# Kernel tuning notes

Measured on AMD Instinct MI355X. Metric: run time of the kernel, lower is better.

Reference implementation:

```python
import jax, jax.numpy as jnp
import numpy as np


def setup_inputs() -> dict:
    key = jax.random.key(0)
    k1, k2 = jax.random.split(key)
    B, H, S, D = 2, 16, 2048, 64
    scores = jax.random.normal(k1, (B, H, S, S), dtype=jnp.float32)
    v = jax.random.normal(k2, (B, H, S, D), dtype=jnp.float32)
    return {"scores": scores, "v": v}


def reference(scores, v):
    # softmax over last dim of [B,H,S,S], then contract with V [B,H,S,D]
    prob = jax.nn.softmax(scores, axis=-1)
    return jnp.einsum('bhqk,bhkd->bhqd', prob, v)
```

## Files before the change

kernel.cpp:

```cpp
#include <hip/hip_runtime.h>
#include <hip/hip_bf16.h>

#define NBH  32
#define SEQ  2048
#define DIM  64
#define PSTR 2056

typedef __attribute__((ext_vector_type(4))) float f32x4;
typedef __attribute__((ext_vector_type(8))) short bf16x8;

__device__ __forceinline__ unsigned short bfbits(float f) {
    unsigned u = __builtin_bit_cast(unsigned, f);
    u += 0x7FFFu + ((u >> 16) & 1u);
    return (unsigned short)(u >> 16);
}
__device__ __forceinline__ unsigned pk(float a, float b) {
    return (unsigned)bfbits(a) | ((unsigned)bfbits(b) << 16);
}

__global__ __launch_bounds__(512, 2)
void softmaxv_kernel(const float* __restrict__ scores,
                     const float* __restrict__ v,
                     float* __restrict__ out)
{
    __shared__ unsigned short P[16 * PSTR];
    __shared__ float red[4][64][8];

    const int tid  = threadIdx.x;
    const int w    = tid >> 6;
    const int lane = tid & 63;
    const int dt   = w & 3;
    const int ksub = w >> 2;
    const int g    = lane >> 4;
    const int c    = lane & 15;

    const int bid = blockIdx.x;
    const int bh  = bid & 31;
    const int s   = bid >> 5;

    const float* sblk = scores + ((size_t)bh * SEQ + s * 256) * SEQ;
    float* const oblk = out + ((size_t)bh * SEQ + s * 256) * DIM;

    bf16x8 ones;
#pragma unroll
    for (int j = 0; j < 8; ++j) ones[j] = (short)0x3F80;

    const int r0 = 2 * w;
    f32x4 st[2][8];

#define SEG(t, rr, j)                                                          \
    (*reinterpret_cast<const f32x4*>(                                          \
        sblk + (size_t)((t) * 16 + r0 + (rr)) * SEQ + (j) * 256 + (lane << 2)))

#define LDS_BAR asm volatile("s_waitcnt lgkmcnt(0)\n\ts_barrier" ::: "memory");

#pragma unroll
    for (int j = 0; j < 8; ++j) { st[0][j] = SEG(0, 0, j); st[1][j] = SEG(0, 1, j); }

    const float* vsrc = v + (size_t)bh * SEQ * DIM + dt * 16 + c;
    bf16x8 vreg[32];
#pragma unroll
    for (int kk = 0; kk < 32; ++kk) {
        bf16x8 f;
#pragma unroll
        for (int j = 0; j < 8; ++j)
            f[j] = (short)bfbits(vsrc[(size_t)(ksub * 1024 + kk * 32 + g * 8 + j) * DIM]);
        vreg[kk] = f;
    }

    for (int t = 0; t < 16; ++t) {
#pragma unroll
        for (int j = 0; j < 8; ++j) {
            const f32x4 sv0 = st[0][j];
            const f32x4 sv1 = st[1][j];
            if (t < 15) {
                st[0][j] = SEG(t + 1, 0, j);
                st[1][j] = SEG(t + 1, 1, j);
            }
            const float a0 = __expf(sv0[0]), a1 = __expf(sv0[1]);
            const float a2 = __expf(sv0[2]), a3 = __expf(sv0[3]);
            const float b0 = __expf(sv1[0]), b1 = __expf(sv1[1]);
            const float b2 = __expf(sv1[2]), b3 = __expf(sv1[3]);
            *reinterpret_cast<uint2*>(&P[r0 * PSTR + j * 256 + lane * 4]) =
                make_uint2(pk(a0, a1), pk(a2, a3));
            *reinterpret_cast<uint2*>(&P[(r0 + 1) * PSTR + j * 256 + lane * 4]) =
                make_uint2(pk(b0, b1), pk(b2, b3));
        }

        LDS_BAR

        f32x4 acc  = (f32x4)0.0f;
        f32x4 accl = (f32x4)0.0f;
#pragma unroll
        for (int kk = 0; kk < 32; ++kk) {
            const int K = ksub * 32 + kk;
            const bf16x8 a = *reinterpret_cast<const bf16x8*>(
                &P[c * PSTR + K * 32 + g * 8]);
            acc  = __builtin_amdgcn_mfma_f32_16x16x32_bf16(a, vreg[kk], acc,  0, 0, 0);
            accl = __builtin_amdgcn_mfma_f32_16x16x32_bf16(a, ones,     accl, 0, 0, 0);
        }

        if (ksub == 1) {
            *reinterpret_cast<f32x4*>(&red[dt][lane][0]) = acc;
            *reinterpret_cast<f32x4*>(&red[dt][lane][4]) = accl;
        }

        LDS_BAR

        if (ksub == 0) {
            const f32x4 a2 = *reinterpret_cast<const f32x4*>(&red[dt][lane][0]);
            const f32x4 l2 = *reinterpret_cast<const f32x4*>(&red[dt][lane][4]);
            const f32x4 at = acc + a2;
            const f32x4 lt = accl + l2;
            float* op = oblk + (size_t)(t * 16) * DIM + dt * 16 + c;
#pragma unroll
            for (int r = 0; r < 4; ++r)
                op[(size_t)(g * 4 + r) * DIM] = at[r] * (1.0f / lt[r]);
        }
    }
#undef SEG
#undef LDS_BAR
}

extern "C" void kernel_launch(void* const* d_in, const int* in_sizes, int n_in,
                              void* d_out, int out_size, void* d_ws, size_t ws_size,
                              hipStream_t stream)
{
    const float* scores = (const float*)d_in[0];
    const float* v      = (const float*)d_in[1];
    float* out          = (float*)d_out;

    softmaxv_kernel<<<dim3(256), dim3(512), 0, stream>>>(scores, v, out);
}
```

Baseline: 114.2 us.

## Double-buffer score loads two tiles ahead with ping-pong register windows

Score prefetch goes from one tile ahead to two tiles ahead, using two register windows (stA/stB) that alternate in a loop unrolled by two. Each window's next load is issued after its pack and barrier, so global loads overlap both the MFMA phase and the next pack. Launch bounds drop to one block per CU so the extra 32 float4 registers fit, which halves occupancy in exchange for deeper memory-level parallelism within each wave.

```diff
diff --git a/kernel.cpp b/kernel.cpp
--- a/kernel.cpp
+++ b/kernel.cpp
@@ -18,7 +18,7 @@
     return (unsigned)bfbits(a) | ((unsigned)bfbits(b) << 16);
 }
 
-__global__ __launch_bounds__(512, 2)
+__global__ __launch_bounds__(512, 1)
 void softmaxv_kernel(const float* __restrict__ scores,
                      const float* __restrict__ v,
                      float* __restrict__ out)
@@ -46,16 +46,71 @@
     for (int j = 0; j < 8; ++j) ones[j] = (short)0x3F80;
 
     const int r0 = 2 * w;
-    f32x4 st[2][8];
+    f32x4 stA[2][8], stB[2][8];
 
 #define SEG(t, rr, j)                                                          \
     (*reinterpret_cast<const f32x4*>(                                          \
         sblk + (size_t)((t) * 16 + r0 + (rr)) * SEQ + (j) * 256 + (lane << 2)))
 
+#define ISSUE_WIN(dst, t)                                                      \
+    {                                                                          \
+        _Pragma("unroll")                                                      \
+        for (int j = 0; j < 8; ++j) {                                          \
+            dst[0][j] = SEG(t, 0, j);                                          \
+            dst[1][j] = SEG(t, 1, j);                                          \
+        }                                                                      \
+    }
+
 #define LDS_BAR asm volatile("s_waitcnt lgkmcnt(0)\n\ts_barrier" ::: "memory");
 
-#pragma unroll
-    for (int j = 0; j < 8; ++j) { st[0][j] = SEG(0, 0, j); st[1][j] = SEG(0, 1, j); }
+#define PACK(src)                                                              \
+    {                                                                          \
+        _Pragma("unroll")                                                      \
+        for (int j = 0; j < 8; ++j) {                                          \
+            const f32x4 sv0 = src[0][j];                                       \
+            const f32x4 sv1 = src[1][j];                                       \
+            const float a0 = __expf(sv0[0]), a1 = __expf(sv0[1]);              \
+            const float a2 = __expf(sv0[2]), a3 = __expf(sv0[3]);              \
+            const float b0 = __expf(sv1[0]), b1 = __expf(sv1[1]);              \
+            const float b2 = __expf(sv1[2]), b3 = __expf(sv1[3]);              \
+            *reinterpret_cast<uint2*>(&P[r0 * PSTR + j * 256 + lane * 4]) =    \
+                make_uint2(pk(a0, a1), pk(a2, a3));                            \
+            *reinterpret_cast<uint2*>(&P[(r0 + 1) * PSTR + j * 256 + lane * 4]) = \
+                make_uint2(pk(b0, b1), pk(b2, b3));                            \
+        }                                                                      \
+    }
+
+#define MFMA_EPI(t)                                                            \
+    {                                                                          \
+        f32x4 acc  = (f32x4)0.0f;                                              \
+        f32x4 accl = (f32x4)0.0f;                                              \
+        _Pragma("unroll")                                                      \
+        for (int kk = 0; kk < 32; ++kk) {                                      \
+            const int K = ksub * 32 + kk;                                      \
+            const bf16x8 a = *reinterpret_cast<const bf16x8*>(                 \
+                &P[c * PSTR + K * 32 + g * 8]);                                \
+            acc  = __builtin_amdgcn_mfma_f32_16x16x32_bf16(a, vreg[kk], acc,  0, 0, 0); \
+            accl = __builtin_amdgcn_mfma_f32_16x16x32_bf16(a, ones,     accl, 0, 0, 0); \
+        }                                                                      \
+        if (ksub == 1) {                                                       \
+            *reinterpret_cast<f32x4*>(&red[dt][lane][0]) = acc;                \
+            *reinterpret_cast<f32x4*>(&red[dt][lane][4]) = accl;               \
+        }                                                                      \
+        LDS_BAR                                                                \
+        if (ksub == 0) {                                                       \
+            const f32x4 a2 = *reinterpret_cast<const f32x4*>(&red[dt][lane][0]); \
+            const f32x4 l2 = *reinterpret_cast<const f32x4*>(&red[dt][lane][4]); \
+            const f32x4 at = acc + a2;                                         \
+            const f32x4 lt = accl + l2;                                        \
+            float* op = oblk + (size_t)((t) * 16) * DIM + dt * 16 + c;         \
+            _Pragma("unroll")                                                  \
+            for (int r = 0; r < 4; ++r)                                        \
+                op[(size_t)(g * 4 + r) * DIM] = at[r] * (1.0f / lt[r]);        \
+        }                                                                      \
+    }
+
+    ISSUE_WIN(stA, 0)
+    ISSUE_WIN(stB, 1)
 
     const float* vsrc = v + (size_t)bh * SEQ * DIM + dt * 16 + c;
     bf16x8 vreg[32];
@@ -68,58 +123,22 @@
         vreg[kk] = f;
     }
 
-    for (int t = 0; t < 16; ++t) {
-#pragma unroll
-        for (int j = 0; j < 8; ++j) {
-            const f32x4 sv0 = st[0][j];
-            const f32x4 sv1 = st[1][j];
-            if (t < 15) {
-                st[0][j] = SEG(t + 1, 0, j);
-                st[1][j] = SEG(t + 1, 1, j);
-            }
-            const float a0 = __expf(sv0[0]), a1 = __expf(sv0[1]);
-            const float a2 = __expf(sv0[2]), a3 = __expf(sv0[3]);
-            const float b0 = __expf(sv1[0]), b1 = __expf(sv1[1]);
-            const float b2 = __expf(sv1[2]), b3 = __expf(sv1[3]);
-            *reinterpret_cast<uint2*>(&P[r0 * PSTR + j * 256 + lane * 4]) =
-                make_uint2(pk(a0, a1), pk(a2, a3));
-            *reinterpret_cast<uint2*>(&P[(r0 + 1) * PSTR + j * 256 + lane * 4]) =
-                make_uint2(pk(b0, b1), pk(b2, b3));
-        }
+    for (int t = 0; t < 16; t += 2) {
+        PACK(stA)
+        LDS_BAR
+        if (t + 2 < 16) ISSUE_WIN(stA, t + 2)
+        MFMA_EPI(t)
 
+        PACK(stB)
         LDS_BAR
-
-        f32x4 acc  = (f32x4)0.0f;
-        f32x4 accl = (f32x4)0.0f;
-#pragma unroll
-        for (int kk = 0; kk < 32; ++kk) {
-            const int K = ksub * 32 + kk;
-            const bf16x8 a = *reinterpret_cast<const bf16x8*>(
-                &P[c * PSTR + K * 32 + g * 8]);
-            acc  = __builtin_amdgcn_mfma_f32_16x16x32_bf16(a, vreg[kk], acc,  0, 0, 0);
-            accl = __builtin_amdgcn_mfma_f32_16x16x32_bf16(a, ones,     accl, 0, 0, 0);
-        }
-
-        if (ksub == 1) {
-            *reinterpret_cast<f32x4*>(&red[dt][lane][0]) = acc;
-            *reinterpret_cast<f32x4*>(&red[dt][lane][4]) = accl;
-        }
-
-        LDS_BAR
-
-        if (ksub == 0) {
-            const f32x4 a2 = *reinterpret_cast<const f32x4*>(&red[dt][lane][0]);
-            const f32x4 l2 = *reinterpret_cast<const f32x4*>(&red[dt][lane][4]);
-            const f32x4 at = acc + a2;
-            const f32x4 lt = accl + l2;
-            float* op = oblk + (size_t)(t * 16) * DIM + dt * 16 + c;
-#pragma unroll
-            for (int r = 0; r < 4; ++r)
-                op[(size_t)(g * 4 + r) * DIM] = at[r] * (1.0f / lt[r]);
-        }
+        if (t + 3 < 16) ISSUE_WIN(stB, t + 3)
+        MFMA_EPI(t + 1)
     }
 #undef SEG
+#undef ISSUE_WIN
 #undef LDS_BAR
+#undef PACK
+#undef MFMA_EPI
 }
 
 extern "C" void kernel_launch(void* const* d_in, const int* in_sizes, int n_in,
```

New measurement: 168.6 us. 47.6% more time.
